# Performance work log

Measured on AMD Instinct MI355X. Metric: run time of the kernel, lower is better.

Reference implementation:

```python
import jax, jax.numpy as jnp
import numpy as np

N_SAMPLES = 524288
N_FEATURES = 64
N_GATES = 64
N_OUTPUTS = 8
BASE = N_FEATURES + 2                # X cols + constant-0 col + constant-1 col
MAX_CONN = BASE + N_GATES            # 130
TEMPERATURE = 1.0                    # forward() default
NEG = -1e9                           # mask value for not-yet-available slots


def setup_inputs() -> dict:
    key = jax.random.key(0)
    k1, k2, k3 = jax.random.split(key, 3)
    X = jax.random.uniform(k1, (N_SAMPLES, N_FEATURES), dtype=jnp.float32)
    gate_weights = jax.random.normal(k2, (N_GATES, MAX_CONN), dtype=jnp.float32) * 0.1
    output_weights = jax.random.normal(k3, (N_GATES, N_OUTPUTS), dtype=jnp.float32) * 0.1
    output_scale = jnp.ones((N_OUTPUTS,), dtype=jnp.float32)
    return {"X": X, "gate_weights": gate_weights,
            "output_weights": output_weights, "output_scale": output_scale}


def reference(X, gate_weights, output_weights, output_scale):
    n = X.shape[0]
    # available = [X | zeros | ones | gate slots]; gate slots filled sequentially
    buf = jnp.concatenate([
        X,
        jnp.zeros((n, 1), X.dtype),
        jnp.ones((n, 1), X.dtype),
        jnp.zeros((n, N_GATES), X.dtype),
    ], axis=1)                                            # [N, MAX_CONN]

    # Connection selection is data-independent: softmax over the first
    # (BASE + gate_idx) slots of each gate's weight row, then top-2.
    col_ids = jnp.arange(MAX_CONN)
    avail_mask = col_ids[None, :] < (BASE + jnp.arange(N_GATES))[:, None]
    logits = jnp.where(avail_mask, gate_weights / TEMPERATURE, NEG)
    probs = jax.nn.softmax(logits, axis=1)                # [n_gates, MAX_CONN]
    _, top2 = jax.lax.top_k(probs, 2)                     # [n_gates, 2]

    # Sequential NAND chain over a small fixed number of gates (structural loop).
    gate_outs = []
    for i in range(N_GATES):
        a = buf[:, top2[i, 0]]                            # [N]
        b = buf[:, top2[i, 1]]
        g = 1.0 - a * b                                   # continuous NAND
        gate_outs.append(g)
        buf = buf.at[:, BASE + i].set(g)

    gate_matrix = jnp.stack(gate_outs, axis=1)            # [N, n_gates]
    outputs = (gate_matrix @ output_weights) * output_scale
    return outputs
```

## Files before the change

### kernel.cpp

```cpp
#include <hip/hip_runtime.h>
#include <hip/hip_fp16.h>

#define N_SAMPLES 524288
#define N_FEATURES 64
#define N_GATES 64
#define N_OUTPUTS 8
#define BASE_COLS 66
#define MAX_CONN 130

#define NWAVES 8
#define MAXW 256
#define GWS_STR 131
#define PAD_SLOT (64 | (64 << 8) | (255 << 16))

typedef float v2f __attribute__((ext_vector_type(2)));

struct __align__(8) H22 { __half2 lo, hi; };

__device__ __forceinline__ void top2_ins(float x, int j, float& v1, int& i1, float& v2, int& i2) {
    bool gt1 = (x > v1) || (x == v1 && j < i1);
    bool gt2 = (x > v2) || (x == v2 && j < i2);
    if (gt1) { v2 = v1; i2 = i1; v1 = x; i1 = j; }
    else if (gt2) { v2 = x; i2 = j; }
}

__global__ __launch_bounds__(256) void plan_kernel(
    const float* __restrict__ gw,
    int* __restrict__ stream)
{
    __shared__ float gws[N_GATES * GWS_STR];
    __shared__ float pv1[4][N_GATES], pv2[4][N_GATES];
    __shared__ int   pi1[4][N_GATES], pi2[4][N_GATES];
    __shared__ int   streamL[NWAVES * MAXW];

    const int tid = threadIdx.x;

    const float4* gw4 = (const float4*)gw;
    for (int k = tid; k < (N_GATES * MAX_CONN) / 4; k += 256) {
        float4 v = gw4[k];
        int base = 4 * k;
        #pragma unroll
        for (int e = 0; e < 4; ++e) {
            int idx = base + e;
            int gi  = idx / MAX_CONN;
            int jj  = idx - gi * MAX_CONN;
            gws[gi * GWS_STR + jj] = (&v.x)[e];
        }
    }
    __syncthreads();

    {
        const int g = tid & 63, s = tid >> 6;
        const int avail = BASE_COLS + g;
        int j0 = s * 33;
        int j1 = j0 + 33; if (j1 > avail) j1 = avail;
        float v1 = -1e30f, v2 = -1e30f;
        int   i1 = 0x7fffffff, i2 = 0x7fffffff;
        const float* w = gws + g * GWS_STR;
        for (int j = j0; j < j1; ++j)
            top2_ins(w[j], j, v1, i1, v2, i2);
        pv1[s][g] = v1; pi1[s][g] = i1;
        pv2[s][g] = v2; pi2[s][g] = i2;
    }
    __syncthreads();

    if (tid >= 64) return;
    const int l = tid;

    float v1 = -1e30f, v2 = -1e30f;
    int   i1 = 0x7fffffff, i2 = 0x7fffffff;
    #pragma unroll
    for (int s = 0; s < 4; ++s) {
        top2_ins(pv1[s][l], pi1[s][l], v1, i1, v2, i2);
        top2_ins(pv2[s][l], pi2[s][l], v1, i1, v2, i2);
    }

    const bool ga = (i1 >= BASE_COLS), gb = (i2 >= BASE_COLS);
    const int  pa = ga ? (i1 - BASE_COLS) : 0;
    const int  pb = gb ? (i2 - BASE_COLS) : 0;
    int lvl = 0;
    bool changed = true;
    while (__any(changed)) {
        int la = __shfl(lvl, pa);
        int lb = __shfl(lvl, pb);
        int nl = lvl;
        if (ga && la + 1 > nl) nl = la + 1;
        if (gb && lb + 1 > nl) nl = lb + 1;
        changed = (nl != lvl);
        lvl = nl;
    }

    for (int q = l; q < NWAVES * MAXW; q += 64) streamL[q] = -2;

    int p_base = 0, assigned = 0;
    int myW = 0, myP = 0;
    for (int L = 0; L < 64 && assigned < 64; ++L) {
        unsigned long long mask = __ballot(lvl == L);
        int c = __popcll(mask);
        if (!c) continue;
        int m  = (c + NWAVES - 1) >> 3;
        int mp = (m + 1) & ~1;
        if (lvl == L) {
            int r = __popcll(mask & ((1ull << l) - 1ull));
            myW = r & 7; myP = p_base + (r >> 3);
        }
        if (l <= mp) {
            int val = (l == mp) ? -1 : PAD_SLOT;
            #pragma unroll
            for (int wv = 0; wv < NWAVES; ++wv)
                streamL[wv * MAXW + p_base + l] = val;
        }
        p_base += mp + 1;
        assigned += c;
    }

    streamL[myW * MAXW + myP] = i1 | (i2 << 8) | (l << 16);

    for (int q = l; q < NWAVES * MAXW; q += 64) stream[q] = streamL[q];
}

__global__ __launch_bounds__(512, 4) void circuit_kernel(
    const float* __restrict__ X,
    const int*   __restrict__ stream,
    const float* __restrict__ ow,
    const float* __restrict__ scale,
    float*       __restrict__ out)
{
    __shared__ H22 buf[128 * 64];

    const int tid = threadIdx.x;
    const int w = tid >> 6, t = tid & 63;
    const long long s0 = (long long)blockIdx.x * 256;

    const int* st = stream + w * MAXW;
    const int sv0 = st[t], sv1 = st[64 + t], sv2 = st[128 + t], sv3 = st[192 + t];

    const float4* Xv = (const float4*)(X + s0 * N_FEATURES);
    #pragma unroll
    for (int k = 0; k < 2; ++k) {
        int q  = k * 512 + tid;
        int c4 = q & 15;
        int j  = q >> 4;
        float4 va = Xv[(4 * j)     * 16 + c4];
        float4 vb = Xv[(4 * j + 1) * 16 + c4];
        float4 vc = Xv[(4 * j + 2) * 16 + c4];
        float4 vd = Xv[(4 * j + 3) * 16 + c4];
        #pragma unroll
        for (int i = 0; i < 4; ++i) {
            int c = 4 * c4 + i;
            H22 v;
            v.lo = __halves2half2(__float2half((&va.x)[i]), __float2half((&vb.x)[i]));
            v.hi = __halves2half2(__float2half((&vc.x)[i]), __float2half((&vd.x)[i]));
            buf[c * 64 + (j ^ c4)] = v;
        }
    }
    __syncthreads();

    const __half2 one2  = __half2half2(__float2half(1.0f));
    const __half2 zero2 = __half2half2(__float2half(0.0f));

    v2f accA[N_OUTPUTS], accB[N_OUTPUTS];
    #pragma unroll
    for (int o = 0; o < N_OUTPUTS; ++o) {
        accA[o].x = 0.0f; accA[o].y = 0.0f;
        accB[o].x = 0.0f; accB[o].y = 0.0f;
    }

    #define FETCH(P) ((P) < 128 \
        ? ((P) < 64  ? __builtin_amdgcn_readlane(sv0, (P))       : __builtin_amdgcn_readlane(sv1, (P) - 64)) \
        : ((P) < 192 ? __builtin_amdgcn_readlane(sv2, (P) - 128) : __builtin_amdgcn_readlane(sv3, (P) - 192)))

    #define RD(e, dst) do {                                                    \
        int _row = ((e) >= BASE_COLS) ? ((e) - 2) : (((e) < 64) ? (e) : 0);    \
        dst = buf[_row * 64 + (t ^ ((_row >> 2) & 15))];                       \
        if ((e) == 64)      { dst.lo = zero2; dst.hi = zero2; }                \
        else if ((e) == 65) { dst.lo = one2;  dst.hi = one2;  }                \
    } while (0)

    int p = 0;
    while (true) {
        int sa = FETCH(p);
        if (sa < 0) {
            ++p;
            if (sa == -1) { __syncthreads(); continue; }
            break;
        }
        int sb = FETCH(p + 1);
        p += 2;

        const int ea0 =  sa        & 255, eb0 = (sa >> 8) & 255, g0 = (sa >> 16) & 255;
        const int ea1 =  sb        & 255, eb1 = (sb >> 8) & 255, g1 = (sb >> 16) & 255;

        H22 a0, b0, a1, b1;
        RD(ea0, a0); RD(eb0, b0); RD(ea1, a1); RD(eb1, b1);

        H22 v0, v1;
        v0.lo = __hfma2(__hneg2(a0.lo), b0.lo, one2);
        v0.hi = __hfma2(__hneg2(a0.hi), b0.hi, one2);
        v1.lo = __hfma2(__hneg2(a1.lo), b1.lo, one2);
        v1.hi = __hfma2(__hneg2(a1.hi), b1.hi, one2);

        if (g0 != 255) {
            int row = 64 + g0;
            buf[row * 64 + (t ^ ((row >> 2) & 15))] = v0;
            v2f glo, ghi;
            glo.x = __low2float(v0.lo); glo.y = __high2float(v0.lo);
            ghi.x = __low2float(v0.hi); ghi.y = __high2float(v0.hi);
            #pragma unroll
            for (int o = 0; o < N_OUTPUTS; ++o) {
                float wt = ow[g0 * N_OUTPUTS + o];
                v2f wv; wv.x = wt; wv.y = wt;
                accA[o] = __builtin_elementwise_fma(glo, wv, accA[o]);
                accB[o] = __builtin_elementwise_fma(ghi, wv, accB[o]);
            }
        }
        if (g1 != 255) {
            int row = 64 + g1;
            buf[row * 64 + (t ^ ((row >> 2) & 15))] = v1;
            v2f glo, ghi;
            glo.x = __low2float(v1.lo); glo.y = __high2float(v1.lo);
            ghi.x = __low2float(v1.hi); ghi.y = __high2float(v1.hi);
            #pragma unroll
            for (int o = 0; o < N_OUTPUTS; ++o) {
                float wt = ow[g1 * N_OUTPUTS + o];
                v2f wv; wv.x = wt; wv.y = wt;
                accA[o] = __builtin_elementwise_fma(glo, wv, accA[o]);
                accB[o] = __builtin_elementwise_fma(ghi, wv, accB[o]);
            }
        }
    }
    #undef FETCH
    #undef RD

    __syncthreads();
    float4* red = (float4*)buf;
    #pragma unroll
    for (int o = 0; o < N_OUTPUTS; ++o) {
        float4 v; v.x = accA[o].x; v.y = accA[o].y; v.z = accB[o].x; v.w = accB[o].y;
        red[w * 512 + o * 64 + t] = v;
    }
    __syncthreads();
    #pragma unroll
    for (int k = 0; k < 4; ++k) {
        int f = k * 512 + tid;
        float4 a = red[f], b = red[f + 2048];
        a.x += b.x; a.y += b.y; a.z += b.z; a.w += b.w; red[f] = a;
    }
    __syncthreads();
    #pragma unroll
    for (int k = 0; k < 2; ++k) {
        int f = k * 512 + tid;
        float4 a = red[f], b = red[f + 1024];
        a.x += b.x; a.y += b.y; a.z += b.z; a.w += b.w; red[f] = a;
    }
    __syncthreads();
    {
        int f = tid;
        float4 a = red[f], b = red[f + 512];
        a.x += b.x; a.y += b.y; a.z += b.z; a.w += b.w; red[f] = a;
    }
    __syncthreads();

    if (w == 0) {
        float sc[N_OUTPUTS];
        #pragma unroll
        for (int o = 0; o < N_OUTPUTS; ++o) sc[o] = scale[o];

        float4 F[N_OUTPUTS];
        #pragma unroll
        for (int o = 0; o < N_OUTPUTS; ++o) {
            F[o] = red[o * 64 + t];
            F[o].x *= sc[o]; F[o].y *= sc[o]; F[o].z *= sc[o]; F[o].w *= sc[o];
        }
        float4* outv = (float4*)(out + (s0 + 4 * t) * N_OUTPUTS);
        #pragma unroll
        for (int i = 0; i < 4; ++i) {
            outv[i * 2 + 0] = make_float4((&F[0].x)[i], (&F[1].x)[i], (&F[2].x)[i], (&F[3].x)[i]);
            outv[i * 2 + 1] = make_float4((&F[4].x)[i], (&F[5].x)[i], (&F[6].x)[i], (&F[7].x)[i]);
        }
    }
}

extern "C" void kernel_launch(void* const* d_in, const int* in_sizes, int n_in,
                              void* d_out, int out_size, void* d_ws, size_t ws_size,
                              hipStream_t stream_)
{
    const float* X     = (const float*)d_in[0];
    const float* gw    = (const float*)d_in[1];
    const float* ow    = (const float*)d_in[2];
    const float* scale = (const float*)d_in[3];
    float* out = (float*)d_out;

    int* stream_ws = (int*)d_ws;

    plan_kernel<<<1, 256, 0, stream_>>>(gw, stream_ws);

    const int blocks = N_SAMPLES / 256;
    circuit_kernel<<<blocks, 512, 0, stream_>>>(X, stream_ws, ow, scale, out);
}
```

Before: 241.2 us.

## Use compact per-wave gate streams and store constant rows in shared memory

The planner now packs each wave's gate list per level without padding slots, so waves process gates one at a time instead of in padded pairs. The constant 0 and 1 columns become real rows in the shared buffer, which removes the per-read index remapping and select branches. The stream shrinks to 192 entries per wave, so one fewer readlane register is needed. The cost is losing the two-gates-per-iteration ILP, and each loop iteration still pays for a readlane and a branch.

```diff
diff --git a/kernel.cpp b/kernel.cpp
--- a/kernel.cpp
+++ b/kernel.cpp
@@ -9,9 +9,8 @@
 #define MAX_CONN 130
 
 #define NWAVES 8
-#define MAXW 256
+#define MAXW 192
 #define GWS_STR 131
-#define PAD_SLOT (64 | (64 << 8) | (255 << 16))
 
 typedef float v2f __attribute__((ext_vector_type(2)));
 
@@ -92,29 +91,34 @@
 
     for (int q = l; q < NWAVES * MAXW; q += 64) streamL[q] = -2;
 
-    int p_base = 0, assigned = 0;
-    int myW = 0, myP = 0;
+    int bases[NWAVES];
+    #pragma unroll
+    for (int w = 0; w < NWAVES; ++w) bases[w] = 0;
+
+    int assigned = 0;
     for (int L = 0; L < 64 && assigned < 64; ++L) {
         unsigned long long mask = __ballot(lvl == L);
         int c = __popcll(mask);
         if (!c) continue;
-        int m  = (c + NWAVES - 1) >> 3;
-        int mp = (m + 1) & ~1;
         if (lvl == L) {
             int r = __popcll(mask & ((1ull << l) - 1ull));
-            myW = r & 7; myP = p_base + (r >> 3);
-        }
-        if (l <= mp) {
-            int val = (l == mp) ? -1 : PAD_SLOT;
+            int myW = r & 7, myI = r >> 3;
+            int base = 0;
             #pragma unroll
-            for (int wv = 0; wv < NWAVES; ++wv)
-                streamL[wv * MAXW + p_base + l] = val;
-        }
-        p_base += mp + 1;
+            for (int w = 0; w < NWAVES; ++w) if (myW == w) base = bases[w];
+            streamL[myW * MAXW + base + myI] = i1 | (i2 << 8) | (l << 16);
+        }
+        if (l < NWAVES) {
+            int cnt = (c > l) ? (((c - 1 - l) >> 3) + 1) : 0;
+            streamL[l * MAXW + bases[l] + cnt] = -1;
+        }
+        #pragma unroll
+        for (int w = 0; w < NWAVES; ++w) {
+            int cnt = (c > w) ? (((c - 1 - w) >> 3) + 1) : 0;
+            bases[w] += cnt + 1;
+        }
         assigned += c;
     }
-
-    streamL[myW * MAXW + myP] = i1 | (i2 << 8) | (l << 16);
 
     for (int q = l; q < NWAVES * MAXW; q += 64) stream[q] = streamL[q];
 }
@@ -126,14 +130,14 @@
     const float* __restrict__ scale,
     float*       __restrict__ out)
 {
-    __shared__ H22 buf[128 * 64];
+    __shared__ H22 buf[130 * 64];
 
     const int tid = threadIdx.x;
     const int w = tid >> 6, t = tid & 63;
     const long long s0 = (long long)blockIdx.x * 256;
 
     const int* st = stream + w * MAXW;
-    const int sv0 = st[t], sv1 = st[64 + t], sv2 = st[128 + t], sv3 = st[192 + t];
+    const int sv0 = st[t], sv1 = st[64 + t], sv2 = st[128 + t];
 
     const float4* Xv = (const float4*)(X + s0 * N_FEATURES);
     #pragma unroll
@@ -154,10 +158,16 @@
             buf[c * 64 + (j ^ c4)] = v;
         }
     }
-    __syncthreads();
-
-    const __half2 one2  = __half2half2(__float2half(1.0f));
-    const __half2 zero2 = __half2half2(__float2half(0.0f));
+    if (tid < 64) {
+        H22 z; z.lo = __half2half2(__float2half(0.0f)); z.hi = z.lo;
+        buf[64 * 64 + tid] = z;
+    } else if (tid < 128) {
+        H22 o1; o1.lo = __half2half2(__float2half(1.0f)); o1.hi = o1.lo;
+        buf[65 * 64 + (tid - 64)] = o1;
+    }
+    __syncthreads();
+
+    const __half2 one2 = __half2half2(__float2half(1.0f));
 
     v2f accA[N_OUTPUTS], accB[N_OUTPUTS];
     #pragma unroll
@@ -166,71 +176,39 @@
         accB[o].x = 0.0f; accB[o].y = 0.0f;
     }
 
-    #define FETCH(P) ((P) < 128 \
-        ? ((P) < 64  ? __builtin_amdgcn_readlane(sv0, (P))       : __builtin_amdgcn_readlane(sv1, (P) - 64)) \
-        : ((P) < 192 ? __builtin_amdgcn_readlane(sv2, (P) - 128) : __builtin_amdgcn_readlane(sv3, (P) - 192)))
-
-    #define RD(e, dst) do {                                                    \
-        int _row = ((e) >= BASE_COLS) ? ((e) - 2) : (((e) < 64) ? (e) : 0);    \
-        dst = buf[_row * 64 + (t ^ ((_row >> 2) & 15))];                       \
-        if ((e) == 64)      { dst.lo = zero2; dst.hi = zero2; }                \
-        else if ((e) == 65) { dst.lo = one2;  dst.hi = one2;  }                \
-    } while (0)
-
     int p = 0;
     while (true) {
-        int sa = FETCH(p);
-        if (sa < 0) {
-            ++p;
-            if (sa == -1) { __syncthreads(); continue; }
+        int sv;
+        if (p < 64)       sv = __builtin_amdgcn_readlane(sv0, p);
+        else if (p < 128) sv = __builtin_amdgcn_readlane(sv1, p - 64);
+        else              sv = __builtin_amdgcn_readlane(sv2, p - 128);
+        ++p;
+        if (sv < 0) {
+            if (sv == -1) { __syncthreads(); continue; }
             break;
         }
-        int sb = FETCH(p + 1);
-        p += 2;
-
-        const int ea0 =  sa        & 255, eb0 = (sa >> 8) & 255, g0 = (sa >> 16) & 255;
-        const int ea1 =  sb        & 255, eb1 = (sb >> 8) & 255, g1 = (sb >> 16) & 255;
-
-        H22 a0, b0, a1, b1;
-        RD(ea0, a0); RD(eb0, b0); RD(ea1, a1); RD(eb1, b1);
-
-        H22 v0, v1;
-        v0.lo = __hfma2(__hneg2(a0.lo), b0.lo, one2);
-        v0.hi = __hfma2(__hneg2(a0.hi), b0.hi, one2);
-        v1.lo = __hfma2(__hneg2(a1.lo), b1.lo, one2);
-        v1.hi = __hfma2(__hneg2(a1.hi), b1.hi, one2);
-
-        if (g0 != 255) {
-            int row = 64 + g0;
-            buf[row * 64 + (t ^ ((row >> 2) & 15))] = v0;
-            v2f glo, ghi;
-            glo.x = __low2float(v0.lo); glo.y = __high2float(v0.lo);
-            ghi.x = __low2float(v0.hi); ghi.y = __high2float(v0.hi);
-            #pragma unroll
-            for (int o = 0; o < N_OUTPUTS; ++o) {
-                float wt = ow[g0 * N_OUTPUTS + o];
-                v2f wv; wv.x = wt; wv.y = wt;
-                accA[o] = __builtin_elementwise_fma(glo, wv, accA[o]);
-                accB[o] = __builtin_elementwise_fma(ghi, wv, accB[o]);
-            }
-        }
-        if (g1 != 255) {
-            int row = 64 + g1;
-            buf[row * 64 + (t ^ ((row >> 2) & 15))] = v1;
-            v2f glo, ghi;
-            glo.x = __low2float(v1.lo); glo.y = __high2float(v1.lo);
-            ghi.x = __low2float(v1.hi); ghi.y = __high2float(v1.hi);
-            #pragma unroll
-            for (int o = 0; o < N_OUTPUTS; ++o) {
-                float wt = ow[g1 * N_OUTPUTS + o];
-                v2f wv; wv.x = wt; wv.y = wt;
-                accA[o] = __builtin_elementwise_fma(glo, wv, accA[o]);
-                accB[o] = __builtin_elementwise_fma(ghi, wv, accB[o]);
-            }
-        }
-    }
-    #undef FETCH
-    #undef RD
+        const int ea = sv & 255, eb = (sv >> 8) & 255, g = (sv >> 16) & 255;
+
+        H22 a = buf[ea * 64 + (t ^ ((ea >> 2) & 15))];
+        H22 b = buf[eb * 64 + (t ^ ((eb >> 2) & 15))];
+
+        H22 v;
+        v.lo = __hfma2(__hneg2(a.lo), b.lo, one2);
+        v.hi = __hfma2(__hneg2(a.hi), b.hi, one2);
+        const int row = 66 + g;
+        buf[row * 64 + (t ^ ((row >> 2) & 15))] = v;
+
+        v2f glo, ghi;
+        glo.x = __low2float(v.lo); glo.y = __high2float(v.lo);
+        ghi.x = __low2float(v.hi); ghi.y = __high2float(v.hi);
+        #pragma unroll
+        for (int o = 0; o < N_OUTPUTS; ++o) {
+            float wt = ow[g * N_OUTPUTS + o];
+            v2f wv; wv.x = wt; wv.y = wt;
+            accA[o] = __builtin_elementwise_fma(glo, wv, accA[o]);
+            accB[o] = __builtin_elementwise_fma(ghi, wv, accB[o]);
+        }
+    }
 
     __syncthreads();
     float4* red = (float4*)buf;
```

New measurement: 233.5 us. 3.2% less time.
